# Performance work log

Hardware: AMD Instinct MI355X
Metric: run time of the kernel (lower is better)

The kernel has to match this reference:

```python
import jax, jax.numpy as jnp
import numpy as np

B, S, DIM, E, TR, G = 2, 896, 1536, 8, 1643, 8
TYPE_RANGES = ((0, 228), (228, 519), (519, 1286), (1286, 1643))
TOPK = 3


def setup_inputs() -> dict:
    key = jax.random.key(0)
    ks = jax.random.split(key, 16)
    w = 0.02  # weight scale to keep activations sane
    return {
        "x": jax.random.normal(ks[0], (B, S, 2 * DIM), jnp.float32),
        "out": jax.random.normal(ks[1], (B, S, TR), jnp.float32),
        "embedding": jax.random.normal(ks[2], (1, 1, DIM), jnp.float32),
        "index": jax.random.permutation(ks[3], TR).astype(jnp.int32),
        "Wsel": jax.random.normal(ks[4], (2 * DIM, G), jnp.float32) * w,
        "bsel": jax.random.normal(ks[5], (G,), jnp.float32) * w,
        "Wemb": jax.random.normal(ks[6], (DIM, G), jnp.float32) * w,
        "bemb": jax.random.normal(ks[7], (G,), jnp.float32) * w,
        "Wg": jax.random.normal(ks[8], (G, S, E), jnp.float32) * w,
        "bg": jax.random.normal(ks[9], (G, E), jnp.float32) * w,
        "temb": jax.random.normal(ks[10], (4, S), jnp.float32),
        "W1": jax.random.normal(ks[11], (E, S, 2 * S), jnp.float32) * w,
        "b1": jax.random.normal(ks[12], (E, 2 * S), jnp.float32) * w,
        "W2": jax.random.normal(ks[13], (E, 2 * S, S), jnp.float32) * w,
        "b2": jax.random.normal(ks[14], (E, S), jnp.float32) * w,
    }


def reference(x, out, embedding, index, Wsel, bsel, Wemb, bemb, Wg, bg, temb, W1, b1, W2, b2):
    Bb, Ss, Tr = out.shape
    # gate selector inputs: mean-pool x over sequence (AdaptiveAvgPool1d(1))
    gate_logits = x.mean(axis=1) @ Wsel + bsel            # (B, G)
    emb_logits = embedding[:, 0, :] @ Wemb + bemb          # (1, G)
    residual = out
    o = jnp.swapaxes(out, 1, 2)[:, index, :]               # (B, TR, S), gathered track order

    gates_list, weights_list = [], []
    zloss = jnp.zeros((), out.dtype)
    for i, (s0, s1) in enumerate(TYPE_RANGES):
        T = s1 - s0
        temp = (o[:, s0:s1, :] + temb[i]).reshape(Bb * T, Ss)
        tok = gate_logits[:, 2 * i:2 * i + 2]              # (B, 2)
        embl = emb_logits[:, 2 * i:2 * i + 2]              # (1, 2)
        w2 = (jax.nn.softmax(tok, axis=-1) + jax.nn.softmax(embl, axis=-1)) / 2.0  # (B, 2)
        zloss = zloss + jnp.mean(tok ** 2) + jnp.mean(embl ** 2)
        g = jnp.zeros((Bb, T, E), out.dtype)
        for j in range(2):
            logits = jax.nn.leaky_relu(temp @ Wg[2 * i + j] + bg[2 * i + j])  # (B*T, E)
            zloss = zloss + jnp.mean(logits ** 2)
            topv, topi = jax.lax.top_k(logits, TOPK)
            probs = jax.nn.softmax(topv, axis=-1)
            tg = jnp.zeros_like(logits).at[jnp.arange(Bb * T)[:, None], topi].set(probs)
            g = g + tg.reshape(Bb, T, E) * w2[:, j][:, None, None]
        gates_list.append(g)
        weights_list.append(jax.lax.stop_gradient(w2))
    gates = jnp.concatenate(gates_list, axis=1)            # (B, TR, E)
    weights = jnp.concatenate(weights_list, axis=1)        # (B, 8)
    all_gates = jnp.stack([gates[:, s0:s1, :].reshape(-1, E).sum(0) for s0, s1 in TYPE_RANGES])  # (4, E)

    # dense-equivalent of gather -> grouped GEMM -> scatter-add combine
    gf = gates.reshape(Bb * Tr, E)
    xf = o.reshape(Bb * Tr, Ss)
    h = jax.nn.relu(jnp.einsum('ns,esh->neh', xf, W1) + b1[None])  # (N, E, 2S)
    oe = jnp.einsum('neh,ehs->nes', h, W2) + b2[None]              # (N, E, S)
    y = jnp.einsum('ne,nes->ns', gf, oe).reshape(Bb, Tr, Ss)
    yfull = jnp.zeros((Bb, Tr, Ss), out.dtype).at[:, index, :].set(y)
    y_out = jnp.swapaxes(yfull, 1, 2) + residual
    return (y_out, all_gates, zloss, jnp.zeros((), out.dtype), weights)
```

## Files before the change

kernel.cpp:

```cpp
#include <hip/hip_runtime.h>

typedef unsigned short u16;
typedef unsigned int u32;
typedef __bf16 bf16x8 __attribute__((ext_vector_type(8)));
typedef float f32x4 __attribute__((ext_vector_type(4)));

#define S_    896
#define TR_   1643
#define NTOK_ 3286
#define MP_   3328

__device__ __forceinline__ u16 f2bf(float f) {
  u32 u = __builtin_bit_cast(u32, f);
  u = (u + 0x7FFFu + ((u >> 16) & 1u)) >> 16;
  return (u16)u;
}

__device__ __forceinline__ void gload16(const void* g, void* l) {
  __builtin_amdgcn_global_load_lds(
      (const __attribute__((address_space(1))) u32*)g,
      (__attribute__((address_space(3))) u32*)l, 16, 0, 0);
}

__global__ void k_init(const int* __restrict__ index, int* __restrict__ inv,
                       float* __restrict__ xmean, float* __restrict__ o32,
                       u16* __restrict__ obf, float* __restrict__ gf) {
  int i = blockIdx.x * 256 + threadIdx.x;
  if (i < TR_) inv[index[i]] = i;
  if (i < 6144) xmean[i] = 0.f;
  if (i < 336) gf[(size_t)NTOK_ * 8 + i] = 0.f;
  o32[(size_t)NTOK_ * S_ + i] = 0.f;
  obf[(size_t)NTOK_ * S_ + i] = 0;
}

__global__ void k_reduce_x(const float* __restrict__ x, float* __restrict__ xmean) {
  int i = blockIdx.x * 256 + threadIdx.x;
  int b = i / 3072, d = i % 3072;
  int s0 = blockIdx.y * 224;
  const float* p = x + (size_t)b * S_ * 3072 + (size_t)s0 * 3072 + d;
  float s = 0.f;
  for (int t = 0; t < 224; ++t) s += p[(size_t)t * 3072];
  atomicAdd(&xmean[i], s * (1.f / (float)S_));
}

__global__ __launch_bounds__(256)
void k_small_dots(const float* __restrict__ xmean,
                  const float* __restrict__ Wsel, const float* __restrict__ bsel,
                  const float* __restrict__ emb,  const float* __restrict__ Wemb,
                  const float* __restrict__ bemb, float* __restrict__ glel) {
  __shared__ float red[256];
  int blk = blockIdx.x, tid = threadIdx.x;
  float s = 0.f;
  if (blk < 16) {
    int b = blk >> 3, g = blk & 7;
    for (int d = tid; d < 3072; d += 256) s += xmean[b * 3072 + d] * Wsel[d * 8 + g];
  } else {
    int g = blk - 16;
    for (int d = tid; d < 1536; d += 256) s += emb[d] * Wemb[d * 8 + g];
  }
  red[tid] = s; __syncthreads();
  for (int st = 128; st > 0; st >>= 1) { if (tid < st) red[tid] += red[tid + st]; __syncthreads(); }
  if (tid == 0) glel[blk] = red[0] + (blk < 16 ? bsel[blk & 7] : bemb[blk - 16]);
}

__global__ void k_small_tail(const float* __restrict__ glel,
                             float* __restrict__ w2buf, float* __restrict__ zpart,
                             float* __restrict__ outw) {
  if (threadIdx.x != 0) return;
  const float* gl = glel;
  const float* el = glel + 16;
  float zp = 0.f;
  for (int i = 0; i < 4; ++i) {
    float e0 = el[2 * i], e1 = el[2 * i + 1];
    float m = fmaxf(e0, e1);
    float x0 = expf(e0 - m), x1 = expf(e1 - m);
    float den = x0 + x1;
    float se0 = x0 / den, se1 = x1 / den;
    zp += (e0 * e0 + e1 * e1) * 0.5f;
    float tsq = 0.f;
    for (int b = 0; b < 2; ++b) {
      float t0 = gl[b * 8 + 2 * i], t1 = gl[b * 8 + 2 * i + 1];
      tsq += t0 * t0 + t1 * t1;
      float mm = fmaxf(t0, t1);
      float y0 = expf(t0 - mm), y1 = expf(t1 - mm);
      float dd = y0 + y1;
      float w0 = (y0 / dd + se0) * 0.5f, w1 = (y1 / dd + se1) * 0.5f;
      w2buf[b * 8 + 2 * i] = w0; w2buf[b * 8 + 2 * i + 1] = w1;
      outw[b * 8 + 2 * i]  = w0; outw[b * 8 + 2 * i + 1]  = w1;
    }
    zp += tsq * 0.25f;
  }
  *zpart = zp;
}

__global__ __launch_bounds__(256)
void k_gather(const float* __restrict__ out_in, const int* __restrict__ inv,
              float* __restrict__ o32, u16* __restrict__ obf) {
  __shared__ float tile[32][33];
  int b = blockIdx.z;
  int tr0 = blockIdx.x * 32, s0 = blockIdx.y * 32;
  int tx = threadIdx.x & 31, ty = threadIdx.x >> 5;
  int ntr = TR_ - tr0; if (ntr > 32) ntr = 32;
  for (int i = ty; i < 32; i += 8)
    tile[i][tx] = (tx < ntr) ? out_in[((size_t)b * S_ + s0 + i) * TR_ + tr0 + tx] : 0.f;
  __syncthreads();
  for (int r = ty; r < ntr; r += 8) {
    int t = inv[tr0 + r];
    size_t off = ((size_t)b * TR_ + t) * S_ + s0 + tx;
    float v = tile[tx][r];
    o32[off] = v;
    obf[off] = f2bf(v);
  }
}

__global__ __launch_bounds__(256)
void k_gates(const float* __restrict__ o32, const float* __restrict__ temb,
             const float* __restrict__ Wg, const float* __restrict__ bg,
             const float* __restrict__ w2buf, float* __restrict__ gf,
             float* __restrict__ zbuf) {
  int n = blockIdx.x;
  int b = n / TR_, t = n % TR_;
  int typ = (t < 228) ? 0 : (t < 519) ? 1 : (t < 1286) ? 2 : 3;
  int tid = threadIdx.x;
  const float* orow = o32 + (size_t)n * S_;
  const float* trow = temb + typ * S_;
  const float* W0 = Wg + (size_t)(2 * typ) * S_ * 8;

  float acc[16];
#pragma unroll
  for (int k = 0; k < 16; ++k) acc[k] = 0.f;
  for (int s = tid; s < S_; s += 256) {
    float ov = orow[s] + trow[s];
    const float4* wa = (const float4*)(W0 + s * 8);
    const float4* wb = (const float4*)(W0 + 7168 + s * 8);
    float4 a0 = wa[0], a1 = wa[1], b0 = wb[0], b1 = wb[1];
    acc[0]  += ov * a0.x; acc[1]  += ov * a0.y; acc[2]  += ov * a0.z; acc[3]  += ov * a0.w;
    acc[4]  += ov * a1.x; acc[5]  += ov * a1.y; acc[6]  += ov * a1.z; acc[7]  += ov * a1.w;
    acc[8]  += ov * b0.x; acc[9]  += ov * b0.y; acc[10] += ov * b0.z; acc[11] += ov * b0.w;
    acc[12] += ov * b1.x; acc[13] += ov * b1.y; acc[14] += ov * b1.z; acc[15] += ov * b1.w;
  }
#pragma unroll
  for (int k = 0; k < 16; ++k)
#pragma unroll
    for (int m = 1; m < 64; m <<= 1) acc[k] += __shfl_xor(acc[k], m, 64);

  __shared__ float wsum[4][16];
  __shared__ float lgsh[16];
  int w = tid >> 6, lane = tid & 63;
  if (lane == 0)
#pragma unroll
    for (int k = 0; k < 16; ++k) wsum[w][k] = acc[k];
  __syncthreads();
  if (tid < 16)
    lgsh[tid] = wsum[0][tid] + wsum[1][tid] + wsum[2][tid] + wsum[3][tid]
              + bg[(2 * typ + (tid >> 3)) * 8 + (tid & 7)];
  __syncthreads();

  if (tid == 0) {
    float g[8];
    for (int k = 0; k < 8; ++k) g[k] = 0.f;
    float zs[2];
    for (int j = 0; j < 2; ++j) {
      float l[8]; float ss = 0.f;
      for (int k = 0; k < 8; ++k) {
        float v = lgsh[j * 8 + k];
        v = v > 0.f ? v : 0.01f * v;
        l[k] = v; ss += v * v;
      }
      zs[j] = ss;
      int i0 = 0;
      for (int k = 1; k < 8; ++k) if (l[k] > l[i0]) i0 = k;
      int i1 = -1;
      for (int k = 0; k < 8; ++k) { if (k == i0) continue; if (i1 < 0 || l[k] > l[i1]) i1 = k; }
      int i2 = -1;
      for (int k = 0; k < 8; ++k) { if (k == i0 || k == i1) continue; if (i2 < 0 || l[k] > l[i2]) i2 = k; }
      float p1 = expf(l[i1] - l[i0]), p2 = expf(l[i2] - l[i0]);
      float den = 1.f + p1 + p2;
      float w2 = w2buf[b * 8 + 2 * typ + j];
      g[i0] += w2 / den; g[i1] += w2 * p1 / den; g[i2] += w2 * p2 / den;
    }
    float* gfp = gf + (size_t)n * 8;
    for (int k = 0; k < 8; ++k) gfp[k] = g[k];
    zbuf[n * 2 + 0] = zs[0];
    zbuf[n * 2 + 1] = zs[1];
  }
}

__global__ __launch_bounds__(256)
void k_reduce_gates(const float* __restrict__ gf, const float* __restrict__ zbuf,
                    float* __restrict__ allg, float* __restrict__ zsum) {
  __shared__ float red[256];
  const int s0a[4] = {0, 228, 519, 1286};
  const int cta[4] = {228, 291, 767, 357};
  int blk = blockIdx.x, tid = threadIdx.x;
  float s = 0.f;
  if (blk < 32) {
    int typ = blk >> 3, e = blk & 7;
    int s0 = s0a[typ], cnt = cta[typ];
    for (int i = tid; i < 2 * cnt; i += 256) {
      int bb = i / cnt, tt = s0 + i % cnt;
      s += gf[(size_t)(bb * TR_ + tt) * 8 + e];
    }
  } else {
    int idx = blk - 32, typ = idx >> 1, j = idx & 1;
    int s0 = s0a[typ], cnt = cta[typ];
    for (int i = tid; i < 2 * cnt; i += 256) {
      int bb = i / cnt, tt = s0 + i % cnt;
      s += zbuf[(size_t)(bb * TR_ + tt) * 2 + j];
    }
  }
  red[tid] = s; __syncthreads();
  for (int st = 128; st > 0; st >>= 1) { if (tid < st) red[tid] += red[tid + st]; __syncthreads(); }
  if (tid == 0) {
    if (blk < 32) allg[blk] = red[0];
    else          zsum[blk - 32] = red[0];
  }
}

__global__ __launch_bounds__(256)
void k_transpose(const float* __restrict__ W, u16* __restrict__ Wt,
                 int R, int C, int ldo, size_t eo) {
  __shared__ float tile[32][33];
  int e = blockIdx.z;
  const float* Wp = W + (size_t)e * R * C;
  u16* Wtp = Wt + (size_t)e * eo;
  int c0 = blockIdx.x * 32, r0 = blockIdx.y * 32;
  int tx = threadIdx.x & 31, ty = threadIdx.x >> 5;
  for (int i = ty; i < 32; i += 8)
    tile[i][tx] = (c0 + tx < C) ? Wp[(size_t)(r0 + i) * C + c0 + tx] : 0.f;
  __syncthreads();
  for (int i = ty; i < 32; i += 8) Wtp[(size_t)(c0 + i) * ldo + r0 + tx] = f2bf(tile[tx][i]);
}

template <int MODE>
__global__ __launch_bounds__(512, 2)
void k_gemm8(const u16* __restrict__ A, const u16* __restrict__ Bt,
             int K, int lda, int ldb,
             const float* __restrict__ gf, const float* __restrict__ bias,
             u16* __restrict__ H, float* __restrict__ ypart, int P) {
  __shared__ __align__(16) u16 lds[2 * 32768];
  const int tid = threadIdx.x;
  const int lane = tid & 63;
  const int wid = tid >> 6;
  const int wr = wid >> 2, wc = wid & 3;

  int bx, by, bz = 0;
  if (MODE == 1) {
    int f = blockIdx.y * 56 + blockIdx.x;
    f = (f & 7) * 91 + (f >> 3);
    by = f / 56; bx = f % 56;
  } else {
    int f = blockIdx.z * 52 + blockIdx.y * 4 + blockIdx.x;
    int n8 = (52 * P) >> 3;
    f = (f & 7) * n8 + (f >> 3);
    bz = f / 52; int r = f % 52;
    by = r / 4; bx = r % 4;
  }

  int kt0 = 0, ktN = K >> 6;
  if (MODE == 2) {
    int nt = K >> 6;
    kt0 = (bz * nt) / P; ktN = ((bz + 1) * nt) / P;
  }
  const int NT = ktN - kt0;

  const u16* Ag = A + (size_t)(by * 256) * lda;
  const u16* Bg = Bt + (size_t)(bx * 256) * ldb;

#define SA(buf, g, k0)                                                          \
  { _Pragma("unroll")                                                           \
    for (int q = 0; q < 2; ++q) {                                               \
      const int br = q * 128 + (g) * 64 + wid * 8;                              \
      const int row = br + (lane >> 3);                                         \
      gload16(Ag + (size_t)row * lda + (((lane & 7) ^ (lane >> 3)) << 3) + (k0),\
              lds + (buf) * 32768 + br * 64 + lane * 8);                        \
    } }
#define SB(buf, g, k0)                                                          \
  { _Pragma("unroll")                                                           \
    for (int q = 0; q < 2; ++q) {                                               \
      const int sI = q * 8 + wid;                                               \
      const int br = (sI >> 2) * 64 + (g) * 32 + (sI & 3) * 8;                  \
      const int row = br + (lane >> 3);                                         \
      gload16(Bg + (size_t)row * ldb + (((lane & 7) ^ (lane >> 3)) << 3) + (k0),\
              lds + (buf) * 32768 + 16384 + br * 64 + lane * 8);                \
    } }
#define PSYNC(N)                                             \
  asm volatile("s_waitcnt vmcnt(" #N ")" ::: "memory");      \
  __builtin_amdgcn_s_barrier();                              \
  __builtin_amdgcn_sched_barrier(0);

  const int l15 = lane & 15, l16 = lane >> 4, l7 = lane & 7;
  const int swz0 = (l16 ^ l7) << 3;
  const int swz1 = ((4 + l16) ^ l7) << 3;
  const int rA = (wr * 128 + l15) * 64;
  const int rB = (wc * 64 + l15) * 64;

  f32x4 acc[8][4] = {};
  bf16x8 aF[4][2], b0F[2][2], b1F[2][2];

#define READ_A0  _Pragma("unroll") for (int i = 0; i < 4; ++i) {               \
    aF[i][0] = *(const bf16x8*)(lA + rA + i * 1024 + swz0);                    \
    aF[i][1] = *(const bf16x8*)(lA + rA + i * 1024 + swz1); }
#define READ_A1  _Pragma("unroll") for (int i = 0; i < 4; ++i) {               \
    aF[i][0] = *(const bf16x8*)(lA + rA + (i + 4) * 1024 + swz0);              \
    aF[i][1] = *(const bf16x8*)(lA + rA + (i + 4) * 1024 + swz1); }
#define READ_B0  _Pragma("unroll") for (int j = 0; j < 2; ++j) {               \
    b0F[j][0] = *(const bf16x8*)(lB + rB + j * 1024 + swz0);                   \
    b0F[j][1] = *(const bf16x8*)(lB + rB + j * 1024 + swz1); }
#define READ_B1  _Pragma("unroll") for (int j = 0; j < 2; ++j) {               \
    b1F[j][0] = *(const bf16x8*)(lB + rB + (j + 2) * 1024 + swz0);             \
    b1F[j][1] = *(const bf16x8*)(lB + rB + (j + 2) * 1024 + swz1); }
#define MFMA16(IB, JB, BF)                                                     \
  __builtin_amdgcn_s_setprio(1);                                               \
  _Pragma("unroll") for (int i = 0; i < 4; ++i)                                \
  _Pragma("unroll") for (int j = 0; j < 2; ++j) {                              \
    acc[i + IB][j + JB] = __builtin_amdgcn_mfma_f32_16x16x32_bf16(aF[i][0], BF[j][0], acc[i + IB][j + JB], 0, 0, 0); \
    acc[i + IB][j + JB] = __builtin_amdgcn_mfma_f32_16x16x32_bf16(aF[i][1], BF[j][1], acc[i + IB][j + JB], 0, 0, 0); \
  }                                                                            \
  __builtin_amdgcn_s_setprio(0);

  { const int k0 = kt0 << 6; SA(0, 0, k0) SB(0, 0, k0) SB(0, 1, k0) SA(0, 1, k0) }

  int cur = 0;
  for (int t = 0; t < NT - 1; ++t) {
    const u16* lA = lds + cur * 32768;
    const u16* lB = lA + 16384;
    const int nk0 = (kt0 + t + 1) << 6;
    PSYNC(4)
    SA(cur ^ 1, 0, nk0) SB(cur ^ 1, 0, nk0)
    READ_A0 READ_B0
    MFMA16(0, 0, b0F)
    PSYNC(6)
    SB(cur ^ 1, 1, nk0)
    READ_B1
    MFMA16(0, 2, b1F)
    PSYNC(6)
    SA(cur ^ 1, 1, nk0)
    READ_A1
    MFMA16(4, 2, b1F)
    MFMA16(4, 0, b0F)
    cur ^= 1;
  }
  {
    const u16* lA = lds + cur * 32768;
    const u16* lB = lA + 16384;
    PSYNC(4)
    READ_A0 READ_B0
    MFMA16(0, 0, b0F)
    PSYNC(2)
    READ_B1
    MFMA16(0, 2, b1F)
    PSYNC(0)
    READ_A1
    MFMA16(4, 2, b1F)
    MFMA16(4, 0, b0F)
  }
#undef SA
#undef SB
#undef PSYNC
#undef READ_A0
#undef READ_A1
#undef READ_B0
#undef READ_B1
#undef MFMA16

  if (MODE == 1) {
    const int e = bx / 7;
#pragma unroll
    for (int j = 0; j < 4; ++j) {
      const int col = bx * 256 + wc * 64 + j * 16 + l15;
      const float bia = bias[col];
#pragma unroll
      for (int i = 0; i < 8; ++i)
#pragma unroll
        for (int r = 0; r < 4; ++r) {
          const int row = by * 256 + wr * 128 + i * 16 + l16 * 4 + r;
          float v = acc[i][j][r] + bia;
          v = v > 0.f ? v : 0.f;
          H[(size_t)row * 14336 + col] = f2bf(v * gf[row * 8 + e]);
        }
    }
  } else {
    float* yp = ypart + (size_t)bz * ((size_t)MP_ * 1024);
#pragma unroll
    for (int j = 0; j < 4; ++j) {
      const int col = bx * 256 + wc * 64 + j * 16 + l15;
      if (col < 896) {
#pragma unroll
        for (int i = 0; i < 8; ++i)
#pragma unroll
          for (int r = 0; r < 4; ++r) {
            const int row = by * 256 + wr * 128 + i * 16 + l16 * 4 + r;
            yp[(size_t)row * 1024 + col] = acc[i][j][r];
          }
      }
    }
  }
}

__global__ __launch_bounds__(256)
void k_reduce_yT(const float* __restrict__ yp, int P,
                 const float* __restrict__ gf, const float* __restrict__ b2,
                 float* __restrict__ yT) {
  __shared__ float tile[32][33];
  int b = blockIdx.z;
  int t0 = blockIdx.x * 32, s0 = blockIdx.y * 32;
  int tx = threadIdx.x & 31, ty = threadIdx.x >> 5;
  int ntv = TR_ - t0; if (ntv > 32) ntv = 32;
  for (int r = ty; r < 32; r += 8) {
    float acc = 0.f;
    if (r < ntv) {
      size_t n = (size_t)b * TR_ + t0 + r;
      size_t base = n * 1024 + s0 + tx;
      for (int p = 0; p < P; ++p) acc += yp[(size_t)p * ((size_t)MP_ * 1024) + base];
      const float* g = gf + n * 8;
#pragma unroll
      for (int e = 0; e < 8; ++e) acc += g[e] * b2[e * S_ + s0 + tx];
    }
    tile[r][tx] = acc;
  }
  __syncthreads();
  for (int i = ty; i < 32; i += 8)
    if (tx < ntv)
      yT[((size_t)b * S_ + s0 + i) * TR_ + t0 + tx] = tile[tx][i];
}

__global__ void k_scatter(const float* __restrict__ yT, const float* __restrict__ out_in,
                          const int* __restrict__ inv, float* __restrict__ dout,
                          const float* __restrict__ allg, const float* __restrict__ zsum,
                          const float* __restrict__ zpart) {
  int i = blockIdx.x * 256 + threadIdx.x;
  int tr = i % TR_;
  dout[i] = out_in[i] + yT[(size_t)(i - tr) + inv[tr]];
  if (blockIdx.x == 0) {
    int tid = threadIdx.x;
    if (tid < 32) dout[2944256 + tid] = allg[tid];
    else if (tid == 32) {
      float z = *zpart;
      const int Ts[4] = {228, 291, 767, 357};
      for (int q = 0; q < 4; ++q)
        for (int j = 0; j < 2; ++j)
          z += zsum[q * 2 + j] / (float)(2 * Ts[q] * 8);
      dout[2944288] = z;
      dout[2944289] = 0.f;
    }
  }
}

extern "C" void kernel_launch(void* const* d_in, const int* in_sizes, int n_in,
                              void* d_out, int out_size, void* d_ws, size_t ws_size,
                              hipStream_t stream) {
  const float* x         = (const float*)d_in[0];
  const float* out_in    = (const float*)d_in[1];
  const float* embedding = (const float*)d_in[2];
  const int*   index     = (const int*)d_in[3];
  const float* Wsel      = (const float*)d_in[4];
  const float* bsel      = (const float*)d_in[5];
  const float* Wemb      = (const float*)d_in[6];
  const float* bemb      = (const float*)d_in[7];
  const float* Wg        = (const float*)d_in[8];
  const float* bg        = (const float*)d_in[9];
  const float* temb      = (const float*)d_in[10];
  const float* W1        = (const float*)d_in[11];
  const float* b1        = (const float*)d_in[12];
  const float* W2        = (const float*)d_in[13];
  const float* b2        = (const float*)d_in[14];
  float* dout = (float*)d_out;

  char* ws = (char*)d_ws;
  float* allg  = (float*)(ws + 0);
  float* zsum  = (float*)(ws + 128);
  float* zpart = (float*)(ws + 160);
  float* w2buf = (float*)(ws + 192);
  int*   inv   = (int*)(ws + 256);
  float* glel  = (float*)(ws + 6912);
  float* xmean = (float*)(ws + 8192);
  float* gf    = (float*)(ws + 32768);
  float* o32   = (float*)(ws + 139264);
  float* yT    = o32;
  float* zbuf  = (float*)(ws + 139264 + (size_t)NTOK_ * S_ * 4);
  u16*   obf   = (u16*)(ws + 12066816);
  u16*   w1t   = (u16*)(ws + 18030592);
  u16*   w2t   = (u16*)(ws + 43720704);
  u16*   Hb    = (u16*)(ws + 73080832);

  const size_t HIGH = 168501248ull, YPSZ = (size_t)MP_ * 1024 * 4;
  int P; float* ypart = (float*)(ws + HIGH);
  if      (ws_size >= HIGH + 8 * YPSZ) P = 8;
  else if (ws_size >= HIGH + 6 * YPSZ) P = 6;
  else if (ws_size >= HIGH + 4 * YPSZ) P = 4;
  else                                 P = 2;

  k_init<<<147, 256, 0, stream>>>(index, inv, xmean, o32, obf, gf);
  k_reduce_x<<<dim3(24, 4), 256, 0, stream>>>(x, xmean);
  k_small_dots<<<24, 256, 0, stream>>>(xmean, Wsel, bsel, embedding, Wemb, bemb, glel);
  k_small_tail<<<1, 64, 0, stream>>>(glel, w2buf, zpart, dout + 2944290);
  k_gather<<<dim3(52, 28, 2), 256, 0, stream>>>(out_in, inv, o32, obf);
  k_gates<<<NTOK_, 256, 0, stream>>>(o32, temb, Wg, bg, w2buf, gf, zbuf);
  k_reduce_gates<<<40, 256, 0, stream>>>(gf, zbuf, allg, zsum);

  k_transpose<<<dim3(56, 28, 8), 256, 0, stream>>>(W1, w1t, 896, 1792, 896, (size_t)1605632);
  k_gemm8<1><<<dim3(56, 13), 512, 0, stream>>>(
      obf, w1t, 896, 896, 896, gf, b1, Hb, nullptr, 0);

  k_transpose<<<dim3(32, 56, 8), 256, 0, stream>>>(W2, w2t, 1792, 896, 14336, (size_t)1792);
  k_gemm8<2><<<dim3(4, 13, P), 512, 0, stream>>>(
      Hb, w2t, 14336, 14336, 14336, nullptr, nullptr, nullptr, ypart, P);
  k_reduce_yT<<<dim3(52, 28, 2), 256, 0, stream>>>(ypart, P, gf, b2, yT);

  k_scatter<<<11501, 256, 0, stream>>>(yT, out_in, inv, dout, allg, zsum, zpart);
}
```

Baseline: 393.4 us.

## Route tokens per expert with compacted lists instead of dense all-expert GEMMs

Builds per-expert compacted token lists from nonzero gate values, gathers only routed token rows into a bf16 per-expert buffer, and runs grouped GEMMs per expert that exit early for empty row tiles. The second GEMM no longer does a K=14336 split-K reduction over all experts; it produces per-expert bf16 outputs that a combine kernel sums through position lookups. The aim is to skip the compute for tokens whose gate is zero, since top-3 of 8 experts per gate pair leaves many zeros. In exchange it adds list-building and gather kernels, a serial prefix scan, and bf16 rounding of the expert outputs before combining.

Result: no change. 389.5 us (-1.0%).

```diff
diff --git a/kernel.cpp b/kernel.cpp
--- a/kernel.cpp
+++ b/kernel.cpp
@@ -4,6 +4,7 @@
 typedef unsigned int u32;
 typedef __bf16 bf16x8 __attribute__((ext_vector_type(8)));
 typedef float f32x4 __attribute__((ext_vector_type(4)));
+typedef u16 u16x8 __attribute__((ext_vector_type(8)));
 
 #define S_    896
 #define TR_   1643
@@ -23,14 +24,10 @@
 }
 
 __global__ void k_init(const int* __restrict__ index, int* __restrict__ inv,
-                       float* __restrict__ xmean, float* __restrict__ o32,
-                       u16* __restrict__ obf, float* __restrict__ gf) {
+                       float* __restrict__ xmean) {
   int i = blockIdx.x * 256 + threadIdx.x;
   if (i < TR_) inv[index[i]] = i;
   if (i < 6144) xmean[i] = 0.f;
-  if (i < 336) gf[(size_t)NTOK_ * 8 + i] = 0.f;
-  o32[(size_t)NTOK_ * S_ + i] = 0.f;
-  obf[(size_t)NTOK_ * S_ + i] = 0;
 }
 
 __global__ void k_reduce_x(const float* __restrict__ x, float* __restrict__ xmean) {
@@ -95,7 +92,7 @@
 
 __global__ __launch_bounds__(256)
 void k_gather(const float* __restrict__ out_in, const int* __restrict__ inv,
-              float* __restrict__ o32, u16* __restrict__ obf) {
+              float* __restrict__ o32) {
   __shared__ float tile[32][33];
   int b = blockIdx.z;
   int tr0 = blockIdx.x * 32, s0 = blockIdx.y * 32;
@@ -106,10 +103,7 @@
   __syncthreads();
   for (int r = ty; r < ntr; r += 8) {
     int t = inv[tr0 + r];
-    size_t off = ((size_t)b * TR_ + t) * S_ + s0 + tx;
-    float v = tile[tx][r];
-    o32[off] = v;
-    obf[off] = f2bf(v);
+    o32[((size_t)b * TR_ + t) * S_ + s0 + tx] = tile[tx][r];
   }
 }
 
@@ -218,6 +212,59 @@
 }
 
 __global__ __launch_bounds__(256)
+void k_build_lists(const float* __restrict__ gf, int* __restrict__ listE,
+                   float* __restrict__ gcomp, int* __restrict__ posT,
+                   int* __restrict__ cntE) {
+  __shared__ int wcnt[4];
+  __shared__ int sbase;
+  int e = blockIdx.x;
+  int tid = threadIdx.x, lane = tid & 63, wv = tid >> 6;
+  if (tid == 0) sbase = 0;
+  __syncthreads();
+  for (int c = 0; c < 13; ++c) {
+    int n = c * 256 + tid;
+    float gv = (n < NTOK_) ? gf[(size_t)n * 8 + e] : 0.f;
+    bool flag = (n < NTOK_) && (gv != 0.f);
+    unsigned long long m = __ballot(flag);
+    if (lane == 0) wcnt[wv] = __popcll(m);
+    __syncthreads();
+    int prefix = 0;
+    for (int w = 0; w < 4; ++w) if (w < wv) prefix += wcnt[w];
+    int within = __popcll(m & ((1ull << lane) - 1ull));
+    if (n < NTOK_) {
+      if (flag) {
+        int idx = sbase + prefix + within;
+        listE[e * MP_ + idx] = n;
+        gcomp[e * MP_ + idx] = gv;
+        posT[(size_t)n * 8 + e] = idx;
+      } else {
+        posT[(size_t)n * 8 + e] = -1;
+      }
+    }
+    __syncthreads();
+    if (tid == 0) sbase += wcnt[0] + wcnt[1] + wcnt[2] + wcnt[3];
+    __syncthreads();
+  }
+  if (tid == 0) cntE[e] = sbase;
+}
+
+__global__ void k_gatherE(const float* __restrict__ o32, const int* __restrict__ listE,
+                          const int* __restrict__ cntE, u16* __restrict__ obfE) {
+  int idx = blockIdx.x * 256 + threadIdx.x;
+  int g = idx / 112, w8 = (idx % 112) * 8;
+  int e = g / MP_, i = g % MP_;
+  if (i >= cntE[e]) return;
+  int n = listE[g];
+  const float* src = o32 + (size_t)n * S_ + w8;
+  float4 v0 = *(const float4*)src;
+  float4 v1 = *(const float4*)(src + 4);
+  u16x8 o;
+  o[0] = f2bf(v0.x); o[1] = f2bf(v0.y); o[2] = f2bf(v0.z); o[3] = f2bf(v0.w);
+  o[4] = f2bf(v1.x); o[5] = f2bf(v1.y); o[6] = f2bf(v1.z); o[7] = f2bf(v1.w);
+  *(u16x8*)(obfE + (size_t)g * S_ + w8) = o;
+}
+
+__global__ __launch_bounds__(256)
 void k_transpose(const float* __restrict__ W, u16* __restrict__ Wt,
                  int R, int C, int ldo, size_t eo) {
   __shared__ float tile[32][33];
@@ -234,38 +281,34 @@
 
 template <int MODE>
 __global__ __launch_bounds__(512, 2)
-void k_gemm8(const u16* __restrict__ A, const u16* __restrict__ Bt,
-             int K, int lda, int ldb,
-             const float* __restrict__ gf, const float* __restrict__ bias,
-             u16* __restrict__ H, float* __restrict__ ypart, int P) {
+void k_gemm8s(const u16* __restrict__ A, const u16* __restrict__ Bt,
+              const int* __restrict__ cntE,
+              const float* __restrict__ gcomp, const float* __restrict__ bias,
+              u16* __restrict__ H, u16* __restrict__ Ye) {
   __shared__ __align__(16) u16 lds[2 * 32768];
   const int tid = threadIdx.x;
   const int lane = tid & 63;
   const int wid = tid >> 6;
   const int wr = wid >> 2, wc = wid & 3;
 
-  int bx, by, bz = 0;
-  if (MODE == 1) {
-    int f = blockIdx.y * 56 + blockIdx.x;
-    f = (f & 7) * 91 + (f >> 3);
-    by = f / 56; bx = f % 56;
-  } else {
-    int f = blockIdx.z * 52 + blockIdx.y * 4 + blockIdx.x;
-    int n8 = (52 * P) >> 3;
-    f = (f & 7) * n8 + (f >> 3);
-    bz = f / 52; int r = f % 52;
-    by = r / 4; bx = r % 4;
-  }
-
-  int kt0 = 0, ktN = K >> 6;
-  if (MODE == 2) {
-    int nt = K >> 6;
-    kt0 = (bz * nt) / P; ktN = ((bz + 1) * nt) / P;
-  }
-  const int NT = ktN - kt0;
-
-  const u16* Ag = A + (size_t)(by * 256) * lda;
-  const u16* Bg = Bt + (size_t)(bx * 256) * ldb;
+  const int K   = (MODE == 1) ? 896 : 1792;
+  const int lda = K, ldb = K;
+  const int nx  = (MODE == 1) ? 7 : 4;
+  const int n8  = (MODE == 1) ? 91 : 52;
+  const size_t bes = (MODE == 1) ? 1605632u : 1835008u;
+
+  int f0 = (blockIdx.z * 13 + blockIdx.y) * nx + blockIdx.x;
+  int f = (f0 & 7) * n8 + (f0 >> 3);
+  const int ez = f / n8;
+  const int r8 = f % n8;
+  const int by = r8 / nx, bx = r8 % nx;
+
+  const int cnt = cntE[ez];
+  if (by * 256 >= cnt) return;
+
+  const u16* Ag = A + ((size_t)ez * MP_ + (size_t)by * 256) * lda;
+  const u16* Bg = Bt + (size_t)ez * bes + (size_t)(bx * 256) * ldb;
+  const int NT = K >> 6;
 
 #define SA(buf, g, k0)                                                          \
   { _Pragma("unroll")                                                           \
@@ -319,13 +362,13 @@
   }                                                                            \
   __builtin_amdgcn_s_setprio(0);
 
-  { const int k0 = kt0 << 6; SA(0, 0, k0) SB(0, 0, k0) SB(0, 1, k0) SA(0, 1, k0) }
+  SA(0, 0, 0) SB(0, 0, 0) SB(0, 1, 0) SA(0, 1, 0)
 
   int cur = 0;
   for (int t = 0; t < NT - 1; ++t) {
     const u16* lA = lds + cur * 32768;
     const u16* lB = lA + 16384;
-    const int nk0 = (kt0 + t + 1) << 6;
+    const int nk0 = (t + 1) << 6;
     PSYNC(4)
     SA(cur ^ 1, 0, nk0) SB(cur ^ 1, 0, nk0)
     READ_A0 READ_B0
@@ -365,11 +408,10 @@
 #undef MFMA16
 
   if (MODE == 1) {
-    const int e = bx / 7;
 #pragma unroll
     for (int j = 0; j < 4; ++j) {
       const int col = bx * 256 + wc * 64 + j * 16 + l15;
-      const float bia = bias[col];
+      const float bia = bias[ez * 1792 + col];
 #pragma unroll
       for (int i = 0; i < 8; ++i)
 #pragma unroll
@@ -377,11 +419,10 @@
           const int row = by * 256 + wr * 128 + i * 16 + l16 * 4 + r;
           float v = acc[i][j][r] + bia;
           v = v > 0.f ? v : 0.f;
-          H[(size_t)row * 14336 + col] = f2bf(v * gf[row * 8 + e]);
+          H[((size_t)ez * MP_ + row) * 1792 + col] = f2bf(v * gcomp[ez * MP_ + row]);
         }
     }
   } else {
-    float* yp = ypart + (size_t)bz * ((size_t)MP_ * 1024);
 #pragma unroll
     for (int j = 0; j < 4; ++j) {
       const int col = bx * 256 + wc * 64 + j * 16 + l15;
@@ -391,7 +432,7 @@
 #pragma unroll
           for (int r = 0; r < 4; ++r) {
             const int row = by * 256 + wr * 128 + i * 16 + l16 * 4 + r;
-            yp[(size_t)row * 1024 + col] = acc[i][j][r];
+            Ye[((size_t)ez * MP_ + row) * 896 + col] = f2bf(acc[i][j][r]);
           }
       }
     }
@@ -399,9 +440,9 @@
 }
 
 __global__ __launch_bounds__(256)
-void k_reduce_yT(const float* __restrict__ yp, int P,
-                 const float* __restrict__ gf, const float* __restrict__ b2,
-                 float* __restrict__ yT) {
+void k_combine(const u16* __restrict__ YeE, const int* __restrict__ posT,
+               const float* __restrict__ gf, const float* __restrict__ b2,
+               float* __restrict__ yT) {
   __shared__ float tile[32][33];
   int b = blockIdx.z;
   int t0 = blockIdx.x * 32, s0 = blockIdx.y * 32;
@@ -411,11 +452,18 @@
     float acc = 0.f;
     if (r < ntv) {
       size_t n = (size_t)b * TR_ + t0 + r;
-      size_t base = n * 1024 + s0 + tx;
-      for (int p = 0; p < P; ++p) acc += yp[(size_t)p * ((size_t)MP_ * 1024) + base];
+      const int* pp = posT + n * 8;
       const float* g = gf + n * 8;
-#pragma unroll
-      for (int e = 0; e < 8; ++e) acc += g[e] * b2[e * S_ + s0 + tx];
+      int s = s0 + tx;
+#pragma unroll
+      for (int e = 0; e < 8; ++e) {
+        int p = pp[e];
+        if (p >= 0) {
+          u32 hv = YeE[((size_t)e * MP_ + p) * 896 + s];
+          acc += __builtin_bit_cast(float, hv << 16);
+        }
+        acc += g[e] * b2[e * 896 + s];
+      }
     }
     tile[r][tx] = acc;
   }
@@ -474,39 +522,38 @@
   float* w2buf = (float*)(ws + 192);
   int*   inv   = (int*)(ws + 256);
   float* glel  = (float*)(ws + 6912);
+  int*   cntE  = (int*)(ws + 7040);
   float* xmean = (float*)(ws + 8192);
   float* gf    = (float*)(ws + 32768);
   float* o32   = (float*)(ws + 139264);
   float* yT    = o32;
   float* zbuf  = (float*)(ws + 139264 + (size_t)NTOK_ * S_ * 4);
-  u16*   obf   = (u16*)(ws + 12066816);
-  u16*   w1t   = (u16*)(ws + 18030592);
-  u16*   w2t   = (u16*)(ws + 43720704);
-  u16*   Hb    = (u16*)(ws + 73080832);
-
-  const size_t HIGH = 168501248ull, YPSZ = (size_t)MP_ * 1024 * 4;
-  int P; float* ypart = (float*)(ws + HIGH);
-  if      (ws_size >= HIGH + 8 * YPSZ) P = 8;
-  else if (ws_size >= HIGH + 6 * YPSZ) P = 6;
-  else if (ws_size >= HIGH + 4 * YPSZ) P = 4;
-  else                                 P = 2;
-
-  k_init<<<147, 256, 0, stream>>>(index, inv, xmean, o32, obf, gf);
+  int*   posT  = (int*)(ws + 12066816);
+  int*   listE = (int*)(ws + 12171968);
+  float* gcomp = (float*)(ws + 12278464);
+  u16*   w1t   = (u16*)(ws + 12386304);
+  u16*   w2tE  = (u16*)(ws + 38076416);
+  u16*   obfE  = (u16*)(ws + 67436544);
+  u16*   YeE   = obfE;
+  u16*   HbE   = (u16*)(ws + 115146752);
+
+  k_init<<<26, 256, 0, stream>>>(index, inv, xmean);
   k_reduce_x<<<dim3(24, 4), 256, 0, stream>>>(x, xmean);
   k_small_dots<<<24, 256, 0, stream>>>(xmean, Wsel, bsel, embedding, Wemb, bemb, glel);
   k_small_tail<<<1, 64, 0, stream>>>(glel, w2buf, zpart, dout + 2944290);
-  k_gather<<<dim3(52, 28, 2), 256, 0, stream>>>(out_in, inv, o32, obf);
+  k_gather<<<dim3(52, 28, 2), 256, 0, stream>>>(out_in, inv, o32);
   k_gates<<<NTOK_, 256, 0, stream>>>(o32, temb, Wg, bg, w2buf, gf, zbuf);
   k_reduce_gates<<<40, 256, 0, stream>>>(gf, zbuf, allg, zsum);
 
+  k_build_lists<<<8, 256, 0, stream>>>(gf, listE, gcomp, posT, cntE);
+  k_gatherE<<<11648, 256, 0, stream>>>(o32, listE, cntE, obfE);
+
   k_transpose<<<dim3(56, 28, 8), 256, 0, stream>>>(W1, w1t, 896, 1792, 896, (size_t)1605632);
-  k_gemm8<1><<<dim3(56, 13), 512, 0, stream>>>(
-      obf, w1t, 896, 896, 896, gf, b1, Hb, nullptr, 0);
-
-  k_transpose<<<dim3(32, 56, 8), 256, 0, stream>>>(W2, w2t, 1792, 896, 14336, (size_t)1792);
-  k_gemm8<2><<<dim3(4, 13, P), 512, 0, stream>>>(
-      Hb, w2t, 14336, 14336, 14336, nullptr, nullptr, nullptr, ypart, P);
-  k_reduce_yT<<<dim3(52, 28, 2), 256, 0, stream>>>(ypart, P, gf, b2, yT);
-
+  k_gemm8s<1><<<dim3(7, 13, 8), 512, 0, stream>>>(obfE, w1t, cntE, gcomp, b1, HbE, nullptr);
+
+  k_transpose<<<dim3(32, 56, 8), 256, 0, stream>>>(W2, w2tE, 1792, 896, 1792, (size_t)1835008);
+  k_gemm8s<2><<<dim3(4, 13, 8), 512, 0, stream>>>(HbE, w2tE, cntE, nullptr, nullptr, nullptr, YeE);
+
+  k_combine<<<dim3(52, 28, 2), 256, 0, stream>>>(YeE, posT, gf, b2, yT);
   k_scatter<<<11501, 256, 0, stream>>>(yT, out_in, inv, dout, allg, zsum, zpart);
 }
```
